# Kernel tuning notes

Hardware: AMD Instinct MI355X
Metric: run time of the kernel (lower is better)

Reference implementation:

```python
import jax, jax.numpy as jnp
import numpy as np

N_E = 16384
E_DIM = 64
BETA = 0.25


def setup_inputs() -> dict:
    key = jax.random.key(0)
    k1, k2 = jax.random.split(key)
    z = jax.random.normal(k1, (8, E_DIM, 32, 32), dtype=jnp.float32)
    # original inits uniform(-1/n_e, 1/n_e); use same scale
    emb_w = jax.random.uniform(k2, (N_E, E_DIM), dtype=jnp.float32,
                               minval=-1.0 / N_E, maxval=1.0 / N_E)
    return {"z": z, "emb_w": emb_w}


def reference(z, emb_w):
    # b c h w -> b h w c
    zp = jnp.transpose(z, (0, 2, 3, 1))              # [B,H,W,C]
    zf = zp.reshape(-1, E_DIM)                       # [N, e_dim]

    # pairwise squared distances: ||z||^2 + ||e||^2 - 2 z e^T
    d = (jnp.sum(zf * zf, axis=1, keepdims=True)
         + jnp.sum(emb_w * emb_w, axis=1)
         - 2.0 * jnp.einsum('nd,kd->nk', zf, emb_w))  # [N, n_e]
    idx = jnp.argmin(d, axis=1)                      # [N] int

    # usage tracking (codebook_usage starts at zeros each fresh module)
    usage = jnp.zeros((N_E,), dtype=jnp.float32).at[idx].max(1.0)
    num_unique = jnp.sum(usage).astype(jnp.int32)
    total_usage = jnp.sum(usage) / N_E

    z_q = emb_w[idx].reshape(zp.shape)               # [B,H,W,C]

    # legacy loss: ||sg(z_q)-z||^2 + beta*||z_q-sg(z)||^2
    loss = (jnp.mean((jax.lax.stop_gradient(z_q) - zp) ** 2)
            + BETA * jnp.mean((z_q - jax.lax.stop_gradient(zp)) ** 2))

    # straight-through estimator
    z_q = zp + jax.lax.stop_gradient(z_q - zp)
    z_q = jnp.transpose(z_q, (0, 3, 1, 2))           # b h w c -> b c h w

    return (z_q, loss, idx, num_unique, usage, total_usage)
```

## Files before the change

### kernel.cpp

```cpp
#include <hip/hip_runtime.h>
#include <math.h>

#define N_ROWS 8192
#define N_E    16384
#define EDIM   64
#define KSPLIT 16
#define KPER   1024
#define CHUNK  64
#define NCH    (KPER/CHUNK)

#define OFF_ZQ    0
#define OFF_LOSS  524288
#define OFF_IDX   524289
#define OFF_NUNIQ 532481
#define OFF_USAGE 532482
#define OFF_TOTAL 548866

typedef __attribute__((ext_vector_type(8)))  short  short8;
typedef __attribute__((ext_vector_type(8)))  ushort ushort8;
typedef __attribute__((ext_vector_type(4)))  float  f32x4;

__device__ ushort g_eh[N_E * EDIM];
__device__ ushort g_zh[N_ROWS * EDIM];
__device__ float  g_zt[N_ROWS * EDIM];

__device__ __forceinline__ ushort bf16hi(float v) {
    unsigned u = __float_as_uint(v);
    return (ushort)((u + 0x7fffu + ((u >> 16) & 1u)) >> 16);
}

__global__ __launch_bounds__(256) void vq_split(
    const float* __restrict__ z, const float* __restrict__ emb,
    float* __restrict__ anorm, float* __restrict__ out,
    float* __restrict__ lossacc, unsigned* __restrict__ done)
{
    __shared__ float lds[64][129];
    int bid = blockIdx.x, t = threadIdx.x;
    if (bid < 1024) {
        int i = bid * 256 + t;
        float4 v = ((const float4*)emb)[i];
        ushort4 h;
        h.x = bf16hi(v.x); h.y = bf16hi(v.y);
        h.z = bf16hi(v.z); h.w = bf16hi(v.w);
        ((ushort4*)g_eh)[i] = h;
    } else if (bid < 1088) {
        int zb = bid - 1024;
        int b = zb >> 3, hw0 = (zb & 7) << 7;
        const float* zp = z + (size_t)b * 65536 + hw0;
        for (int i = 0; i < 32; i++) {
            int j = i * 256 + t;
            int d = j >> 7, hw = j & 127;
            lds[d][hw] = zp[d * 1024 + hw];
        }
        __syncthreads();
        for (int i = 0; i < 4; i++) {
            int task = i * 256 + t;
            int hw = task >> 3, oct = task & 7;
            ushort8 h8; float4 f0, f1;
            float* fp0 = (float*)&f0; float* fp1 = (float*)&f1;
#pragma unroll
            for (int q = 0; q < 8; q++) {
                float v = lds[oct * 8 + q][hw];
                ((ushort*)&h8)[q] = bf16hi(v);
                if (q < 4) fp0[q] = v; else fp1[q - 4] = v;
            }
            size_t ro = (size_t)(b * 1024 + hw0 + hw) * 64 + oct * 8;
            *(ushort8*)(g_zh + ro) = h8;
            *(float4*)(g_zt + ro) = f0;
            *(float4*)(g_zt + ro + 4) = f1;
        }
        if (t < 128) {
            double s = 0.0;
            for (int d = 0; d < 64; d++) {
                float v = lds[d][t];
                s += (double)(v * v);
            }
            anorm[b * 1024 + hw0 + t] = (float)s;
        }
    } else {
        int i = (bid - 1088) * 256 + t;
        out[OFF_USAGE + i] = 0.f;
        if (bid == 1088 && t == 0) { *lossacc = 0.f; *done = 0u; }
    }
}

__global__ __launch_bounds__(128) void vq_mfma(const float* __restrict__ anorm,
                                               unsigned* __restrict__ pcand)
{
    __shared__ __align__(16) ushort ebuf[2][8][CHUNK][8];

    const int t = threadIdx.x;
    const int w = t >> 6, lane = t & 63;
    const int rb = blockIdx.x >> 4, split = blockIdx.x & 15;
    const int n0 = rb * 128;
    const int nw = n0 + w * 64;
    const int kbase = split * KPER;
    const int col = lane & 15, quad = lane >> 4;

    short8 ah[4][2];
#pragma unroll
    for (int rt = 0; rt < 4; rt++)
#pragma unroll
        for (int s = 0; s < 2; s++) {
            size_t off = (size_t)(nw + rt * 16 + col) * 64 + s * 32 + quad * 8;
            ah[rt][s] = *(const short8*)(g_zh + off);
        }

    float av[16];
#pragma unroll
    for (int rt = 0; rt < 4; rt++)
#pragma unroll
        for (int r = 0; r < 4; r++)
            av[rt * 4 + r] = anorm[nw + rt * 16 + quad * 4 + r];

    unsigned p1[16], p2[16];
#pragma unroll
    for (int s = 0; s < 16; s++) { p1[s] = 0xFFFFFFFFu; p2[s] = 0xFFFFFFFFu; }

    auto stage = [&](int dbuf, int code0) {
#pragma unroll
        for (int jj = 0; jj < 4; jj++) {
            int g = w * 4 + jj;
            const ushort* ga = g_eh + (size_t)(code0 + lane) * 64 + g * 8;
            __builtin_amdgcn_global_load_lds(
                (const __attribute__((address_space(1))) void*)ga,
                (__attribute__((address_space(3))) void*)&ebuf[dbuf][g][0][0],
                16, 0, 0);
        }
    };

    stage(0, kbase);
    for (int ch = 0; ch < NCH; ch++) {
        int cur = ch & 1;
        if (ch + 1 < NCH) {
            stage(cur ^ 1, kbase + (ch + 1) * CHUNK);
            asm volatile("s_waitcnt vmcnt(4)" ::: "memory");
        } else {
            asm volatile("s_waitcnt vmcnt(0)" ::: "memory");
        }
        __builtin_amdgcn_s_barrier();
        asm volatile("" ::: "memory");
#pragma unroll
        for (int ct = 0; ct < 4; ct++) {
            int cn = ct * 16 + col;
            f32x4 a[4] = {{0,0,0,0},{0,0,0,0},{0,0,0,0},{0,0,0,0}};
#pragma unroll
            for (int s = 0; s < 2; s++) {
                short8 bh = *(const short8*)&ebuf[cur][s * 4 + quad][cn][0];
                a[0] = __builtin_amdgcn_mfma_f32_16x16x32_bf16(ah[0][s], bh, a[0], 0, 0, 0);
                a[1] = __builtin_amdgcn_mfma_f32_16x16x32_bf16(ah[1][s], bh, a[1], 0, 0, 0);
                a[2] = __builtin_amdgcn_mfma_f32_16x16x32_bf16(ah[2][s], bh, a[2], 0, 0, 0);
                a[3] = __builtin_amdgcn_mfma_f32_16x16x32_bf16(ah[3][s], bh, a[3], 0, 0, 0);
            }
            unsigned slot = (unsigned)(ch * 4 + ct);
#pragma unroll
            for (int rt = 0; rt < 4; rt++)
#pragma unroll
                for (int r = 0; r < 4; r++) {
                    int s = rt * 4 + r;
                    float dq = fmaf(-2.0f, a[rt][r], av[s]);
                    unsigned e = (__float_as_uint(dq) << 6) | slot;
                    unsigned hi = (p1[s] > e) ? p1[s] : e;
                    p1[s] = (p1[s] < e) ? p1[s] : e;
                    p2[s] = (p2[s] < hi) ? p2[s] : hi;
                }
        }
        __builtin_amdgcn_s_barrier();
        asm volatile("" ::: "memory");
    }

    unsigned* sc = (unsigned*)ebuf;
#pragma unroll
    for (int s = 0; s < 16; s++) {
        int rt = s >> 2, r = s & 3;
        int lr = w * 64 + rt * 16 + quad * 4 + r;
        unsigned av26 = __float_as_uint(av[s]) & 0x03FFFFFFu;
#pragma unroll
        for (int j = 0; j < 2; j++) {
            unsigned p = j ? p2[s] : p1[s];
            unsigned dq26 = p >> 6;
            int diff = ((int)((dq26 - av26) << 6)) >> 6;
            unsigned packed = ((unsigned)(diff + 32768) << 10)
                            | ((p & 63u) << 4) | (unsigned)col;
            sc[lr * 32 + ((col * 2 + j + lr * 2) & 31)] = packed;
        }
    }
    __syncthreads();
    {
        unsigned b0 = ~0u, b1 = ~0u, b2 = ~0u, b3 = ~0u;
        for (int q = 0; q < 32; q++) {
            unsigned v = sc[t * 32 + ((q + 2 * t) & 31)];
            unsigned m0 = (b0 > v) ? b0 : v;  b0 = (b0 < v) ? b0 : v;
            unsigned m1 = (b1 > m0) ? b1 : m0; b1 = (b1 < m0) ? b1 : m0;
            unsigned m2 = (b2 > m1) ? b2 : m1; b2 = (b2 < m1) ? b2 : m1;
            b3 = (b3 < m2) ? b3 : m2;
        }
        size_t base = (size_t)(n0 + t) * (KSPLIT * 4) + split * 4;
        pcand[base + 0] = b0; pcand[base + 1] = b1;
        pcand[base + 2] = b2; pcand[base + 3] = b3;
    }
}

__device__ __forceinline__ double shfl_xor_d(double p, int m) {
    int2 u = __builtin_bit_cast(int2, p);
    u.x = __shfl_xor(u.x, m);
    u.y = __shfl_xor(u.y, m);
    return __builtin_bit_cast(double, u);
}
__device__ __forceinline__ unsigned long long shfl_xor_u64(unsigned long long p, int m) {
    int2 u = __builtin_bit_cast(int2, p);
    u.x = __shfl_xor(u.x, m);
    u.y = __shfl_xor(u.y, m);
    return __builtin_bit_cast(unsigned long long, u);
}

__global__ __launch_bounds__(256) void vq_refine(
    const float* __restrict__ emb, const float* __restrict__ anorm,
    const unsigned* __restrict__ pcand,
    float* __restrict__ out, int* __restrict__ idxfin)
{
    int t = threadIdx.x;
    int lane = t & 63;
    int n = blockIdx.x * 4 + (t >> 6);
    int li = lane & 15;
    int qd = lane >> 4;

    float4 zf = *(const float4*)(g_zt + (size_t)n * 64 + li * 4);
    double z0 = (double)zf.x, z1 = (double)zf.y;
    double z2 = (double)zf.z, z3 = (double)zf.w;

    float av = anorm[n];
    unsigned av_b = __float_as_uint(av);

    unsigned v = pcand[(size_t)n * 64 + lane];
    unsigned dqb = av_b + (v >> 10) - 32768u;
    float cd = __uint_as_float(dqb);
    int ck = (lane >> 2) * KPER + (int)((v >> 4) & 63u) * 16 + (int)(v & 15u);

    float mn = cd;
#pragma unroll
    for (int s = 1; s < 64; s <<= 1) mn = fminf(mn, __shfl_xor(mn, s));
    float margin = __uint_as_float(av_b & 0xFF800000u) * 0x1p-18f;
    unsigned long long msk = __ballot(cd <= mn + margin);

    unsigned long long bkey = ~0ull;
    while (msk) {
        int ls[4];
#pragma unroll
        for (int j = 0; j < 4; j++) {
            ls[j] = msk ? (__ffsll((unsigned long long)msk) - 1) : -1;
            if (msk) msk &= msk - 1;
        }
        int lsel = ls[qd];
        int lsafe = (lsel >= 0) ? lsel : 0;
        int kq = __shfl(ck, lsafe);
        int k = (lsel >= 0) ? kq : -1;
        double s = 0.0;
        if (k >= 0) {
            float4 ef = *(const float4*)(emb + (size_t)k * EDIM + li * 4);
            s = fma(z3, (double)ef.w,
                fma(z2, (double)ef.z,
                fma(z1, (double)ef.y, z0 * (double)ef.x)));
        }
        s += shfl_xor_d(s, 1);
        s += shfl_xor_d(s, 2);
        s += shfl_xor_d(s, 4);
        s += shfl_xor_d(s, 8);
        if (k >= 0) {
            float c32 = (float)s;
            float dq = av - 2.0f * c32;
            unsigned long long key =
                ((unsigned long long)__float_as_uint(dq) << 32) | (unsigned)k;
            bkey = (key < bkey) ? key : bkey;
        }
    }
#pragma unroll
    for (int m = 1; m < 64; m <<= 1) {
        unsigned long long o = shfl_xor_u64(bkey, m);
        bkey = (o < bkey) ? o : bkey;
    }
    if (lane == 0) {
        int bk = (int)(unsigned)(bkey & 0xffffffffu);
        idxfin[n] = bk;
        out[OFF_IDX + n] = (float)bk;
        out[OFF_USAGE + bk] = 1.0f;
    }
}

__global__ __launch_bounds__(256) void vq_gather(
    const float* __restrict__ z, const float* __restrict__ emb,
    const int* __restrict__ idxfin, float* __restrict__ out,
    float* __restrict__ lossacc, unsigned* __restrict__ done)
{
    __shared__ float buf[32][65];
    __shared__ float red[4];
    __shared__ unsigned lastflag;
    int t = threadIdx.x, w = t >> 6, lane = t & 63;
    int n0 = blockIdx.x * 32;
    int b = n0 >> 10, hw0 = n0 & 1023;
    for (int rr = 0; rr < 8; rr++) {
        int rl = w * 8 + rr;
        int k = idxfin[n0 + rl];
        buf[rl][lane] = emb[(size_t)k * 64 + lane];
    }
    __syncthreads();
    float ls = 0.f;
    int hw_i = t & 31, c0 = t >> 5;
    for (int cc = 0; cc < 8; cc++) {
        int c = c0 * 8 + cc;
        int o = b * 65536 + c * 1024 + hw0 + hw_i;
        float zq = buf[hw_i][c];
        float zv = z[o];
        out[OFF_ZQ + o] = zq;
        float d = zq - zv;
        ls = fmaf(d, d, ls);
    }
#pragma unroll
    for (int s = 1; s < 64; s <<= 1) ls += __shfl_xor(ls, s);
    if (lane == 0) red[w] = ls;
    __syncthreads();
    if (t == 0) {
        atomicAdd(lossacc, red[0] + red[1] + red[2] + red[3]);
        __threadfence();
        unsigned old = atomicAdd(done, 1u);
        lastflag = (old == 255u) ? 1u : 0u;
    }
    __syncthreads();
    if (lastflag) {
        float s = 0.f;
        for (int i = 0; i < 64; i++) s += out[OFF_USAGE + t + i * 256];
#pragma unroll
        for (int sh = 1; sh < 64; sh <<= 1) s += __shfl_xor(s, sh);
        if (lane == 0) red[w] = s;
        __syncthreads();
        if (t == 0) {
            __threadfence();
            float total = atomicAdd(lossacc, 0.0f);
            float cnt = red[0] + red[1] + red[2] + red[3];
            out[OFF_NUNIQ] = cnt;
            out[OFF_TOTAL] = cnt / 16384.0f;
            out[OFF_LOSS]  = total * 1.25f / 524288.0f;
        }
    }
}

extern "C" void kernel_launch(void* const* d_in, const int* in_sizes, int n_in,
                              void* d_out, int out_size, void* d_ws, size_t ws_size,
                              hipStream_t stream)
{
    const float* z   = (const float*)d_in[0];
    const float* emb = (const float*)d_in[1];
    float* out = (float*)d_out;
    char* ws = (char*)d_ws;

    float*    anorm   = (float*)ws;
    unsigned* pcand   = (unsigned*)(ws + 32768);
    int*      idxfin  = (int*)(ws + 32768 + 2097152);
    float*    lossacc = (float*)(ws + 32768 + 2097152 + 32768);
    unsigned* done    = (unsigned*)(ws + 32768 + 2097152 + 32768 + 4);

    vq_split <<<1152, 256, 0, stream>>>(z, emb, anorm, out, lossacc, done);
    vq_mfma  <<<(N_ROWS / 128) * KSPLIT, 128, 0, stream>>>(anorm, pcand);
    vq_refine<<<N_ROWS / 4, 256, 0, stream>>>(emb, anorm, pcand, out, idxfin);
    vq_gather<<<256, 256, 0, stream>>>(z, emb, idxfin, out, lossacc, done);
}
```

Baseline: 124.0 us.

## Give each wave a private LDS codebook buffer to drop block barriers

The MFMA distance kernel grows to 256 threads and 256 rows per block. Each of the four waves now stages the whole 64-code chunk into its own double-buffered LDS region, so the two s_barriers per chunk go away. A single __syncthreads remains before the top-2 candidate scatter. The MFMA accumulation is also unrolled with a zero initial accumulator. The cost is four times the LDS footprint (64 KB per block), which cuts occupancy, and each wave issues redundant global-to-LDS loads of the same codebook data. Fewer, larger blocks also mean less parallelism across the grid.

```diff
diff --git a/kernel.cpp b/kernel.cpp
--- a/kernel.cpp
+++ b/kernel.cpp
@@ -84,15 +84,15 @@
     }
 }
 
-__global__ __launch_bounds__(128) void vq_mfma(const float* __restrict__ anorm,
+__global__ __launch_bounds__(256) void vq_mfma(const float* __restrict__ anorm,
                                                unsigned* __restrict__ pcand)
 {
-    __shared__ __align__(16) ushort ebuf[2][8][CHUNK][8];
+    __shared__ __align__(16) ushort ebuf[4][2][8][CHUNK][8];
 
     const int t = threadIdx.x;
     const int w = t >> 6, lane = t & 63;
     const int rb = blockIdx.x >> 4, split = blockIdx.x & 15;
-    const int n0 = rb * 128;
+    const int n0 = rb * 256;
     const int nw = n0 + w * 64;
     const int kbase = split * KPER;
     const int col = lane & 15, quad = lane >> 4;
@@ -119,56 +119,60 @@
 
     auto stage = [&](int dbuf, int code0) {
 #pragma unroll
-        for (int jj = 0; jj < 4; jj++) {
-            int g = w * 4 + jj;
+        for (int g = 0; g < 8; g++) {
             const ushort* ga = g_eh + (size_t)(code0 + lane) * 64 + g * 8;
             __builtin_amdgcn_global_load_lds(
                 (const __attribute__((address_space(1))) void*)ga,
-                (__attribute__((address_space(3))) void*)&ebuf[dbuf][g][0][0],
+                (__attribute__((address_space(3))) void*)&ebuf[w][dbuf][g][0][0],
                 16, 0, 0);
         }
     };
 
+    const f32x4 Z = {0.f, 0.f, 0.f, 0.f};
     stage(0, kbase);
     for (int ch = 0; ch < NCH; ch++) {
         int cur = ch & 1;
         if (ch + 1 < NCH) {
             stage(cur ^ 1, kbase + (ch + 1) * CHUNK);
-            asm volatile("s_waitcnt vmcnt(4)" ::: "memory");
+            asm volatile("s_waitcnt vmcnt(8)" ::: "memory");
         } else {
             asm volatile("s_waitcnt vmcnt(0)" ::: "memory");
         }
-        __builtin_amdgcn_s_barrier();
-        asm volatile("" ::: "memory");
 #pragma unroll
         for (int ct = 0; ct < 4; ct++) {
             int cn = ct * 16 + col;
-            f32x4 a[4] = {{0,0,0,0},{0,0,0,0},{0,0,0,0},{0,0,0,0}};
-#pragma unroll
-            for (int s = 0; s < 2; s++) {
-                short8 bh = *(const short8*)&ebuf[cur][s * 4 + quad][cn][0];
-                a[0] = __builtin_amdgcn_mfma_f32_16x16x32_bf16(ah[0][s], bh, a[0], 0, 0, 0);
-                a[1] = __builtin_amdgcn_mfma_f32_16x16x32_bf16(ah[1][s], bh, a[1], 0, 0, 0);
-                a[2] = __builtin_amdgcn_mfma_f32_16x16x32_bf16(ah[2][s], bh, a[2], 0, 0, 0);
-                a[3] = __builtin_amdgcn_mfma_f32_16x16x32_bf16(ah[3][s], bh, a[3], 0, 0, 0);
-            }
+            short8 bh0 = *(const short8*)&ebuf[w][cur][quad][cn][0];
+            short8 bh1 = *(const short8*)&ebuf[w][cur][4 + quad][cn][0];
+            f32x4 a0, a1, a2, a3;
+            a0 = __builtin_amdgcn_mfma_f32_16x16x32_bf16(ah[0][0], bh0, Z, 0, 0, 0);
+            a1 = __builtin_amdgcn_mfma_f32_16x16x32_bf16(ah[1][0], bh0, Z, 0, 0, 0);
+            a2 = __builtin_amdgcn_mfma_f32_16x16x32_bf16(ah[2][0], bh0, Z, 0, 0, 0);
+            a3 = __builtin_amdgcn_mfma_f32_16x16x32_bf16(ah[3][0], bh0, Z, 0, 0, 0);
+            a0 = __builtin_amdgcn_mfma_f32_16x16x32_bf16(ah[0][1], bh1, a0, 0, 0, 0);
+            a1 = __builtin_amdgcn_mfma_f32_16x16x32_bf16(ah[1][1], bh1, a1, 0, 0, 0);
+            a2 = __builtin_amdgcn_mfma_f32_16x16x32_bf16(ah[2][1], bh1, a2, 0, 0, 0);
+            a3 = __builtin_amdgcn_mfma_f32_16x16x32_bf16(ah[3][1], bh1, a3, 0, 0, 0);
+
             unsigned slot = (unsigned)(ch * 4 + ct);
-#pragma unroll
-            for (int rt = 0; rt < 4; rt++)
-#pragma unroll
-                for (int r = 0; r < 4; r++) {
+            float dqv;
+#pragma unroll
+            for (int r = 0; r < 4; r++) {
+#pragma unroll
+                for (int rt = 0; rt < 4; rt++) {
                     int s = rt * 4 + r;
-                    float dq = fmaf(-2.0f, a[rt][r], av[s]);
-                    unsigned e = (__float_as_uint(dq) << 6) | slot;
+                    float c = (rt == 0) ? a0[r] : (rt == 1) ? a1[r]
+                            : (rt == 2) ? a2[r] : a3[r];
+                    dqv = fmaf(-2.0f, c, av[s]);
+                    unsigned e = (__float_as_uint(dqv) << 6) | slot;
                     unsigned hi = (p1[s] > e) ? p1[s] : e;
                     p1[s] = (p1[s] < e) ? p1[s] : e;
                     p2[s] = (p2[s] < hi) ? p2[s] : hi;
                 }
-        }
-        __builtin_amdgcn_s_barrier();
-        asm volatile("" ::: "memory");
-    }
-
+            }
+        }
+    }
+
+    __syncthreads();
     unsigned* sc = (unsigned*)ebuf;
 #pragma unroll
     for (int s = 0; s < 16; s++) {
@@ -360,7 +364,7 @@
     unsigned* done    = (unsigned*)(ws + 32768 + 2097152 + 32768 + 4);
 
     vq_split <<<1152, 256, 0, stream>>>(z, emb, anorm, out, lossacc, done);
-    vq_mfma  <<<(N_ROWS / 128) * KSPLIT, 128, 0, stream>>>(anorm, pcand);
+    vq_mfma  <<<(N_ROWS / 256) * KSPLIT, 256, 0, stream>>>(anorm, pcand);
     vq_refine<<<N_ROWS / 4, 256, 0, stream>>>(emb, anorm, pcand, out, idxfin);
     vq_gather<<<256, 256, 0, stream>>>(z, emb, idxfin, out, lossacc, done);
 }
```

Result: slower. 126.9 us (+2.3%).
